# Optimization experiments

Measured on AMD Instinct MI355X. Metric: run time of the kernel, lower is better.

Reference implementation:

```python
import jax, jax.numpy as jnp
import numpy as np

B, ENC_LEN, DEC_LEN = 4, 1024, 256
ENC_H, DEC_H, ATTN = 1024, 1024, 256


def setup_inputs() -> dict:
    key = jax.random.key(0)
    k1, k2, k3, k4, k5, k6 = jax.random.split(key, 6)
    scale = 0.02
    return {
        "encoded_seq": jax.random.normal(k1, (B, ENC_LEN, ENC_H), jnp.float32),
        "decoder_state": jax.random.normal(k2, (B, DEC_LEN, DEC_H), jnp.float32),
        "input_pad_mask": jnp.ones((B, ENC_LEN), jnp.float32),
        "Wh": jax.random.normal(k3, (ENC_H, ATTN), jnp.float32) * scale,
        "Ws": jax.random.normal(k4, (DEC_H, ATTN), jnp.float32) * scale,
        "bs": jax.random.normal(k5, (ATTN,), jnp.float32) * scale,
        "v": jax.random.normal(k6, (ATTN,), jnp.float32) * scale,
    }


def reference(encoded_seq, decoder_state, input_pad_mask, Wh, Ws, bs, v):
    # projections: [B, dec, A] and [B, enc, A]
    proj_dec = jnp.einsum('bdh,ha->bda', decoder_state, Ws) + bs
    proj_enc = jnp.einsum('beh,ha->bea', encoded_seq, Wh)
    # additive score: tanh(broadcast add) then dot with selector vector v
    added = jnp.tanh(proj_dec[:, :, None, :] + proj_enc[:, None, :, :])  # [B,dec,enc,A]
    attn_logits = jnp.einsum('bdea,a->bde', added, v)                    # [B,dec,enc]
    attn_weights = jax.nn.softmax(attn_logits, axis=-1)
    attn_weights2 = attn_weights * input_pad_mask[:, None, :]
    attn_renorm = attn_weights2 / jnp.sum(attn_weights2, axis=-1, keepdims=True)
    context = jnp.einsum('bde,beh->bdh', attn_renorm, encoded_seq)       # [B,dec,enc_h]
    return context, attn_renorm
```

## Files before the change

### kernel.cpp

```cpp
#include <hip/hip_runtime.h>
#include <hip/hip_bf16.h>

#define BB 4
#define ENC_LEN 1024
#define DEC_LEN 256
#define ENC_H 1024
#define ATTN_A 256

#define C2F 2.8853900817779268f

typedef short bf16x8 __attribute__((ext_vector_type(8)));
typedef float f32x4 __attribute__((ext_vector_type(4)));
typedef unsigned int u32x2 __attribute__((ext_vector_type(2)));

union Q2D {
  uint4 q;
  u32x2 d[2];
};
union BF8 {
  u32x2 d[2];
  bf16x8 v;
};

static __device__ __forceinline__ unsigned short f2bf(float x) {
  union {
    float f;
    unsigned int u;
  } c;
  c.f = x;
  unsigned int r = c.u + 0x7FFFu + ((c.u >> 16) & 1u);
  return (unsigned short)(r >> 16);
}

__global__ __launch_bounds__(256) void prep_k(
    const float* __restrict__ Wh, const float* __restrict__ Ws,
    const float* __restrict__ enc, const float* __restrict__ dec,
    unsigned short* __restrict__ WhT, unsigned short* __restrict__ WsT,
    unsigned short* __restrict__ encT, unsigned short* __restrict__ encB,
    unsigned short* __restrict__ decB) {
  __shared__ unsigned short T[64][68];
  const int wb = blockIdx.x;
  const int t = threadIdx.x;
  const int lr = t >> 4;
  const int lc4 = (t & 15) * 4;

  if (wb >= 1152) {
    const int q = wb - 1152;
    const int r0 = (q >> 4) * 64;
    const int c0 = (q & 15) * 64;
#pragma unroll
    for (int p = 0; p < 4; ++p) {
      const int r = lr + p * 16;
      const float4 v = *(const float4*)&dec[(long)(r0 + r) * ENC_H + c0 + lc4];
      ushort4 o;
      o.x = f2bf(v.x);
      o.y = f2bf(v.y);
      o.z = f2bf(v.z);
      o.w = f2bf(v.w);
      *(ushort4*)&decB[(long)(r0 + r) * ENC_H + c0 + lc4] = o;
    }
    return;
  }

  const float* in;
  unsigned short* out;
  unsigned short* out2 = nullptr;
  int R, C, bx, by;
  if (wb < 128) {
    in = (wb < 64) ? Wh : Ws;
    out = (wb < 64) ? WhT : WsT;
    const int tt = wb & 63;
    R = ENC_H;
    C = ATTN_A;
    bx = tt & 3;
    by = tt >> 2;
  } else {
    const int tt0 = wb - 128;
    const int b = tt0 >> 8;
    const int tt = tt0 & 255;
    in = enc + (long)b * ENC_LEN * ENC_H;
    out = encT + (long)b * ENC_H * ENC_LEN;
    out2 = encB + (long)b * ENC_LEN * ENC_H;
    R = ENC_LEN;
    C = ENC_H;
    bx = tt & 15;
    by = tt >> 4;
  }
  const int r0 = by * 64;
  const int c0 = bx * 64;

#pragma unroll
  for (int p = 0; p < 4; ++p) {
    const int r = lr + p * 16;
    const float4 v = *(const float4*)&in[(long)(r0 + r) * C + c0 + lc4];
    ushort4 o;
    o.x = f2bf(v.x);
    o.y = f2bf(v.y);
    o.z = f2bf(v.z);
    o.w = f2bf(v.w);
    *(ushort4*)&T[r][lc4] = o;
    if (out2) *(ushort4*)&out2[(long)(r0 + r) * C + c0 + lc4] = o;
  }
  __syncthreads();
#pragma unroll
  for (int p = 0; p < 4; ++p) {
    const int c = lr + p * 16;
    ushort4 o;
    o.x = T[lc4 + 0][c];
    o.y = T[lc4 + 1][c];
    o.z = T[lc4 + 2][c];
    o.w = T[lc4 + 3][c];
    *(ushort4*)&out[(long)(c0 + c) * R + r0 + lc4] = o;
  }
}

__global__ __launch_bounds__(256) void pgemm(const unsigned short* __restrict__ decB,
                                             const unsigned short* __restrict__ encB,
                                             const unsigned short* __restrict__ WsT,
                                             const unsigned short* __restrict__ WhT,
                                             float* __restrict__ pdP,
                                             float* __restrict__ peP) {
  __shared__ unsigned short As[64][36];
  __shared__ unsigned short Bs[64][36];
  __shared__ float Cs[64][68];

  const int s = blockIdx.z;
  const bool isPD = blockIdx.y < 16;
  const unsigned short* A = isPD ? decB : encB;
  const unsigned short* BT = isPD ? WsT : WhT;
  const int m0 = (isPD ? blockIdx.y : (blockIdx.y - 16)) * 64;
  const int n0 = blockIdx.x * 64;
  const int kb = s * 512;

  const int tid = threadIdx.x;
  const int lane = tid & 63;
  const int wave = tid >> 6;
  const int quad = lane >> 4;
  const int l16 = lane & 15;
  const int wm = (wave >> 1) * 32;
  const int wn = (wave & 1) * 32;
  const int sr = tid >> 2;
  const int sk = (tid & 3) * 8;

  f32x4 acc[2][2] = {{{0.f, 0.f, 0.f, 0.f}, {0.f, 0.f, 0.f, 0.f}},
                     {{0.f, 0.f, 0.f, 0.f}, {0.f, 0.f, 0.f, 0.f}}};

  const unsigned short* Ap = A + (long)(m0 + sr) * ENC_H + kb + sk;
  const unsigned short* Bp = BT + (long)(n0 + sr) * ENC_H + kb + sk;

  Q2D av, bv;
  av.q = *(const uint4*)(Ap);
  bv.q = *(const uint4*)(Bp);

  for (int k0 = 0; k0 < 512; k0 += 32) {
    __syncthreads();
    *(u32x2*)&As[sr][sk] = av.d[0];
    *(u32x2*)&As[sr][sk + 4] = av.d[1];
    *(u32x2*)&Bs[sr][sk] = bv.d[0];
    *(u32x2*)&Bs[sr][sk + 4] = bv.d[1];
    const int kn = (k0 + 32 < 512) ? (k0 + 32) : 0;
    av.q = *(const uint4*)(Ap + kn);
    bv.q = *(const uint4*)(Bp + kn);
    __syncthreads();

    bf16x8 af[2], bfr[2];
#pragma unroll
    for (int i = 0; i < 2; ++i) {
      BF8 t;
      t.d[0] = *(const u32x2*)&As[wm + i * 16 + l16][quad * 8];
      t.d[1] = *(const u32x2*)&As[wm + i * 16 + l16][quad * 8 + 4];
      af[i] = t.v;
    }
#pragma unroll
    for (int j = 0; j < 2; ++j) {
      BF8 t;
      t.d[0] = *(const u32x2*)&Bs[wn + j * 16 + l16][quad * 8];
      t.d[1] = *(const u32x2*)&Bs[wn + j * 16 + l16][quad * 8 + 4];
      bfr[j] = t.v;
    }
#pragma unroll
    for (int i = 0; i < 2; ++i)
#pragma unroll
      for (int j = 0; j < 2; ++j)
        acc[i][j] = __builtin_amdgcn_mfma_f32_16x16x32_bf16(af[i], bfr[j], acc[i][j],
                                                            0, 0, 0);
  }

  if (isPD) {
    float* out = pdP + (long)s * (1024 * ATTN_A);
#pragma unroll
    for (int j = 0; j < 2; ++j) {
      const int col = n0 + wn + j * 16 + l16;
#pragma unroll
      for (int i = 0; i < 2; ++i) {
        const int row = m0 + wm + i * 16 + quad * 4;
#pragma unroll
        for (int r = 0; r < 4; ++r)
          out[(long)(row + r) * ATTN_A + col] = C2F * acc[i][j][r];
      }
    }
  } else {
    __syncthreads();
#pragma unroll
    for (int i = 0; i < 2; ++i)
#pragma unroll
      for (int j = 0; j < 2; ++j)
#pragma unroll
        for (int r = 0; r < 4; ++r)
          Cs[wn + j * 16 + l16][wm + i * 16 + quad * 4 + r] = C2F * acc[i][j][r];
    __syncthreads();
    const int gb = m0 >> 10;
    const int e0 = m0 & 1023;
    float* out = peP + (long)s * (BB * ATTN_A * ENC_LEN);
#pragma unroll
    for (int p = 0; p < 4; ++p) {
      const int arow = (tid >> 4) + p * 16;
      const int e4 = (tid & 15) * 4;
      const float4 o = *(const float4*)&Cs[arow][e4];
      *(float4*)&out[(long)gb * (ATTN_A * ENC_LEN) + (long)(n0 + arow) * ENC_LEN +
                     e0 + e4] = o;
    }
  }
}

__global__ __launch_bounds__(256) void logits_k(const float* __restrict__ peP,
                                                const float* __restrict__ pdP,
                                                const float* __restrict__ v,
                                                const float* __restrict__ bs,
                                                float* __restrict__ p0,
                                                float* __restrict__ p1) {
  const int tid = threadIdx.x;
  const int e = blockIdx.x * 256 + tid;
  const int d0 = blockIdx.y * 16;
  const int b = blockIdx.z >> 1;
  const int a0 = (blockIdx.z & 1) * 128;

  __shared__ float EdT[16][128];
  __shared__ float vv[128];

  {
    const int a = tid & 127;
    const int dh = tid >> 7;
    const float cb = C2F * bs[a0 + a];
#pragma unroll
    for (int j = 0; j < 8; ++j) {
      const int dd = dh * 8 + j;
      const long idx = (long)(b * DEC_LEN + d0 + dd) * ATTN_A + a0 + a;
      EdT[dd][a] =
          __builtin_amdgcn_exp2f(pdP[idx] + pdP[idx + 1024 * ATTN_A] + cb);
    }
    if (dh == 0) vv[a] = -2.0f * v[a0 + a];
  }
  __syncthreads();

  float acc[16];
#pragma unroll
  for (int i = 0; i < 16; ++i) acc[i] = 0.f;

  const float* pe0 = peP + (long)b * (ATTN_A * ENC_LEN) + (long)a0 * ENC_LEN + e;
  const float* pe1 = pe0 + (long)BB * ATTN_A * ENC_LEN;

  float pn0[4], pn1[4];
#pragma unroll
  for (int u = 0; u < 4; ++u) {
    pn0[u] = pe0[(long)u * ENC_LEN];
    pn1[u] = pe1[(long)u * ENC_LEN];
  }

  for (int a4 = 0; a4 < 128; a4 += 4) {
    float Ee[4];
#pragma unroll
    for (int u = 0; u < 4; ++u) Ee[u] = __builtin_amdgcn_exp2f(pn0[u] + pn1[u]);
    const int an = (a4 + 4 < 128) ? (a4 + 4) : 0;
#pragma unroll
    for (int u = 0; u < 4; ++u) {
      pn0[u] = pe0[(long)(an + u) * ENC_LEN];
      pn1[u] = pe1[(long)(an + u) * ENC_LEN];
    }
    const float4 v4 = *(const float4*)&vv[a4];

#pragma unroll
    for (int dd = 0; dd < 16; ++dd) {
      const float4 ed = *(const float4*)&EdT[dd][a4];
      const float dn0 = fmaf(ed.x, Ee[0], 1.0f);
      const float dn1 = fmaf(ed.y, Ee[1], 1.0f);
      const float dn2 = fmaf(ed.z, Ee[2], 1.0f);
      const float dn3 = fmaf(ed.w, Ee[3], 1.0f);
      const float x12 = dn0 * dn1;
      const float x34 = dn2 * dn3;
      float t1 = v4.x * dn1;
      t1 = fmaf(v4.y, dn0, t1);
      float t2 = v4.z * dn3;
      t2 = fmaf(v4.w, dn2, t2);
      float num = t1 * x34;
      num = fmaf(t2, x12, num);
      const float D = x12 * x34;
      const float r = __builtin_amdgcn_rcpf(D);
      acc[dd] = fmaf(num, r, acc[dd]);
    }
  }

  float* po = (blockIdx.z & 1) ? p1 : p0;
  const long base = ((long)(b * DEC_LEN + d0) * ENC_LEN) + e;
#pragma unroll
  for (int dd = 0; dd < 16; ++dd) po[base + (long)dd * ENC_LEN] = acc[dd];
}

__global__ __launch_bounds__(256) void softmax2_k(float* __restrict__ p0,
                                                  const float* __restrict__ p1,
                                                  const float* __restrict__ mask,
                                                  unsigned short* __restrict__ attnB) {
  const int row = blockIdx.x;
  const int b = row >> 8;
  const int tid = threadIdx.x;
  float* rp = p0 + (long)row * ENC_LEN;
  const float* rq = p1 + (long)row * ENC_LEN;
  const float* mp = mask + b * ENC_LEN;
  unsigned short* rb = attnB + (long)row * ENC_LEN;

  float l[4], m[4];
#pragma unroll
  for (int j = 0; j < 4; ++j) {
    l[j] = rp[tid + 256 * j] + rq[tid + 256 * j];
    m[j] = mp[tid + 256 * j];
  }

  __shared__ float redmax[4];
  __shared__ float redsum[4];
  const int lane = tid & 63;
  const int wid = tid >> 6;

  float tm = fmaxf(fmaxf(l[0], l[1]), fmaxf(l[2], l[3]));
#pragma unroll
  for (int off = 1; off < 64; off <<= 1) tm = fmaxf(tm, __shfl_xor(tm, off, 64));
  if (lane == 0) redmax[wid] = tm;
  __syncthreads();
  const float rmax = fmaxf(fmaxf(redmax[0], redmax[1]), fmaxf(redmax[2], redmax[3]));

  const float LOG2E = 1.4426950408889634f;
  float p[4];
  float ts = 0.f;
#pragma unroll
  for (int j = 0; j < 4; ++j) {
    p[j] = __builtin_amdgcn_exp2f((l[j] - rmax) * LOG2E) * m[j];
    ts += p[j];
  }
#pragma unroll
  for (int off = 1; off < 64; off <<= 1) ts += __shfl_xor(ts, off, 64);
  if (lane == 0) redsum[wid] = ts;
  __syncthreads();
  const float rsum = redsum[0] + redsum[1] + redsum[2] + redsum[3];

  const float inv = 1.0f / rsum;
#pragma unroll
  for (int j = 0; j < 4; ++j) {
    const float w = p[j] * inv;
    rp[tid + 256 * j] = w;
    rb[tid + 256 * j] = f2bf(w);
  }
}

__global__ __launch_bounds__(256) void cgemm(const unsigned short* __restrict__ attnB,
                                             const unsigned short* __restrict__ encT,
                                             float* __restrict__ cP) {
  __shared__ unsigned short As[64][36];
  __shared__ unsigned short Bs[64][36];

  const int b = blockIdx.z >> 1;
  const int s = blockIdx.z & 1;
  const int kb = s * 512;
  const unsigned short* A = attnB + (long)b * DEC_LEN * ENC_LEN;
  const unsigned short* BT = encT + (long)b * ENC_H * ENC_LEN;
  float* C = cP + (long)s * (BB * DEC_LEN * ENC_H) + (long)b * DEC_LEN * ENC_H;

  const int tid = threadIdx.x;
  const int lane = tid & 63;
  const int wave = tid >> 6;
  const int quad = lane >> 4;
  const int l16 = lane & 15;
  const int wm = (wave >> 1) * 32;
  const int wn = (wave & 1) * 32;
  const int m0 = blockIdx.y * 64;
  const int n0 = blockIdx.x * 64;
  const int sr = tid >> 2;
  const int sk = (tid & 3) * 8;

  f32x4 acc[2][2] = {{{0.f, 0.f, 0.f, 0.f}, {0.f, 0.f, 0.f, 0.f}},
                     {{0.f, 0.f, 0.f, 0.f}, {0.f, 0.f, 0.f, 0.f}}};

  const unsigned short* Ap = A + (long)(m0 + sr) * ENC_LEN + kb + sk;
  const unsigned short* Bp = BT + (long)(n0 + sr) * ENC_LEN + kb + sk;

  Q2D av, bv;
  av.q = *(const uint4*)(Ap);
  bv.q = *(const uint4*)(Bp);

  for (int k0 = 0; k0 < 512; k0 += 32) {
    __syncthreads();
    *(u32x2*)&As[sr][sk] = av.d[0];
    *(u32x2*)&As[sr][sk + 4] = av.d[1];
    *(u32x2*)&Bs[sr][sk] = bv.d[0];
    *(u32x2*)&Bs[sr][sk + 4] = bv.d[1];
    const int kn = (k0 + 32 < 512) ? (k0 + 32) : 0;
    av.q = *(const uint4*)(Ap + kn);
    bv.q = *(const uint4*)(Bp + kn);
    __syncthreads();

    bf16x8 af[2], bfr[2];
#pragma unroll
    for (int i = 0; i < 2; ++i) {
      BF8 t;
      t.d[0] = *(const u32x2*)&As[wm + i * 16 + l16][quad * 8];
      t.d[1] = *(const u32x2*)&As[wm + i * 16 + l16][quad * 8 + 4];
      af[i] = t.v;
    }
#pragma unroll
    for (int j = 0; j < 2; ++j) {
      BF8 t;
      t.d[0] = *(const u32x2*)&Bs[wn + j * 16 + l16][quad * 8];
      t.d[1] = *(const u32x2*)&Bs[wn + j * 16 + l16][quad * 8 + 4];
      bfr[j] = t.v;
    }
#pragma unroll
    for (int i = 0; i < 2; ++i)
#pragma unroll
      for (int j = 0; j < 2; ++j)
        acc[i][j] = __builtin_amdgcn_mfma_f32_16x16x32_bf16(af[i], bfr[j], acc[i][j],
                                                            0, 0, 0);
  }

#pragma unroll
  for (int j = 0; j < 2; ++j) {
    const int col = n0 + wn + j * 16 + l16;
#pragma unroll
    for (int i = 0; i < 2; ++i) {
      const int row = m0 + wm + i * 16 + quad * 4;
#pragma unroll
      for (int r = 0; r < 4; ++r) C[(long)(row + r) * ENC_H + col] = acc[i][j][r];
    }
  }
}

__global__ __launch_bounds__(256) void creduce(const float* __restrict__ cP,
                                               float* __restrict__ ctx) {
  const long i = ((long)blockIdx.x * 256 + threadIdx.x) * 4;
  const float4 x = *(const float4*)&cP[i];
  const float4 y = *(const float4*)&cP[i + (long)BB * DEC_LEN * ENC_H];
  float4 o;
  o.x = x.x + y.x;
  o.y = x.y + y.y;
  o.z = x.z + y.z;
  o.w = x.w + y.w;
  *(float4*)&ctx[i] = o;
}

template <int OMODE, bool BIAS>
__global__ __launch_bounds__(256) void gemm64(const float* __restrict__ A,
                                              const float* __restrict__ B,
                                              const float* __restrict__ bias,
                                              float* __restrict__ C,
                                              int K, int lda, int ldb, int ldc,
                                              long sA, long sB, long sC) {
  const int bz = blockIdx.z;
  A += (long)bz * sA;
  B += (long)bz * sB;
  C += (long)bz * sC;

  const int tid = threadIdx.x;
  const int tx = tid & 15;
  const int ty = tid >> 4;

  __shared__ float As2[16][64];
  __shared__ float Bs2[16][64];

  float acc[4][4];
#pragma unroll
  for (int i = 0; i < 4; ++i)
#pragma unroll
    for (int j = 0; j < 4; ++j) acc[i][j] = 0.f;

  const int ar = tid >> 2;
  const int ak4 = (tid & 3) << 2;
  const int br = tid >> 4;
  const int bn4 = (tid & 15) << 2;

  const float* Aload = A + (long)(blockIdx.y * 64 + ar) * lda + ak4;
  const float* Bload = B + (long)br * ldb + blockIdx.x * 64 + bn4;

  for (int k0 = 0; k0 < K; k0 += 16) {
    const float4 av = *(const float4*)(Aload + k0);
    const float4 bv = *(const float4*)(Bload + (long)k0 * ldb);
    __syncthreads();
    As2[ak4 + 0][ar] = av.x;
    As2[ak4 + 1][ar] = av.y;
    As2[ak4 + 2][ar] = av.z;
    As2[ak4 + 3][ar] = av.w;
    *(float4*)&Bs2[br][bn4] = bv;
    __syncthreads();
#pragma unroll
    for (int kk = 0; kk < 16; ++kk) {
      const float4 a4 = *(const float4*)&As2[kk][ty << 2];
      const float4 b4 = *(const float4*)&Bs2[kk][tx << 2];
      const float am[4] = {a4.x, a4.y, a4.z, a4.w};
      const float bn[4] = {b4.x, b4.y, b4.z, b4.w};
#pragma unroll
      for (int i = 0; i < 4; ++i)
#pragma unroll
        for (int j = 0; j < 4; ++j) acc[i][j] = fmaf(am[i], bn[j], acc[i][j]);
    }
  }

  if (OMODE == 0) {
    const int row0 = blockIdx.y * 64 + (ty << 2);
    const int col0 = blockIdx.x * 64 + (tx << 2);
    float4 bb4 = make_float4(0.f, 0.f, 0.f, 0.f);
    if (BIAS) bb4 = *(const float4*)&bias[col0];
#pragma unroll
    for (int i = 0; i < 4; ++i) {
      float4 o;
      o.x = acc[i][0] + bb4.x;
      o.y = acc[i][1] + bb4.y;
      o.z = acc[i][2] + bb4.z;
      o.w = acc[i][3] + bb4.w;
      *(float4*)&C[(long)(row0 + i) * ldc + col0] = o;
    }
  } else {
#pragma unroll
    for (int i = 0; i < 4; ++i) {
      const int gr = blockIdx.y * 64 + (ty << 2) + i;
      const int b = gr >> 10;
      const int e = gr & 1023;
#pragma unroll
      for (int j = 0; j < 4; ++j) {
        const int col = blockIdx.x * 64 + (tx << 2) + j;
        C[(long)b * (ATTN_A * ENC_LEN) + (long)col * ENC_LEN + e] = acc[i][j];
      }
    }
  }
}

__global__ __launch_bounds__(256) void logits_fb(const float* __restrict__ peT,
                                                 const float* __restrict__ pd,
                                                 const float* __restrict__ v,
                                                 float* __restrict__ out) {
  const int tid = threadIdx.x;
  const int e = blockIdx.x * 256 + tid;
  const int d0 = blockIdx.y * 8;
  const int b = blockIdx.z;

  __shared__ float cpd[ATTN_A][8];
  __shared__ float vv[ATTN_A];

  {
    const int a = tid;
#pragma unroll
    for (int dd = 0; dd < 8; ++dd)
      cpd[a][dd] = C2F * pd[((b * DEC_LEN + d0 + dd) * ATTN_A) + a];
    vv[a] = -2.0f * v[a];
  }
  __syncthreads();

  float acc[8] = {0.f, 0.f, 0.f, 0.f, 0.f, 0.f, 0.f, 0.f};
  const float* pe = peT + (long)b * (ATTN_A * ENC_LEN) + e;

  for (int a = 0; a < ATTN_A; a += 4) {
    float pes[4];
#pragma unroll
    for (int u = 0; u < 4; ++u) pes[u] = pe[(long)(a + u) * ENC_LEN];
#pragma unroll
    for (int u = 0; u < 4; ++u) {
      const float cpe = C2F * pes[u];
      const float vu = vv[a + u];
      const float4 c0 = *(const float4*)&cpd[a + u][0];
      const float4 c1 = *(const float4*)&cpd[a + u][4];
      const float cd[8] = {c0.x, c0.y, c0.z, c0.w, c1.x, c1.y, c1.z, c1.w};
#pragma unroll
      for (int dd = 0; dd < 8; ++dd) {
        const float x = cd[dd] + cpe;
        const float ex = __builtin_amdgcn_exp2f(x);
        const float r = __builtin_amdgcn_rcpf(ex + 1.0f);
        acc[dd] = fmaf(vu, r, acc[dd]);
      }
    }
  }

  const long base = ((long)(b * DEC_LEN + d0) * ENC_LEN) + e;
#pragma unroll
  for (int dd = 0; dd < 8; ++dd) out[base + (long)dd * ENC_LEN] = acc[dd];
}

__global__ __launch_bounds__(256) void softmax_fb(float* __restrict__ attn,
                                                  const float* __restrict__ mask) {
  const int row = blockIdx.x;
  const int b = row >> 8;
  const int tid = threadIdx.x;
  float* rp = attn + (long)row * ENC_LEN;
  const float* mp = mask + b * ENC_LEN;

  float l[4], m[4];
#pragma unroll
  for (int j = 0; j < 4; ++j) {
    l[j] = rp[tid + 256 * j];
    m[j] = mp[tid + 256 * j];
  }

  __shared__ float redmax[4];
  __shared__ float redsum[4];
  const int lane = tid & 63;
  const int wid = tid >> 6;

  float tm = fmaxf(fmaxf(l[0], l[1]), fmaxf(l[2], l[3]));
#pragma unroll
  for (int off = 1; off < 64; off <<= 1) tm = fmaxf(tm, __shfl_xor(tm, off, 64));
  if (lane == 0) redmax[wid] = tm;
  __syncthreads();
  const float rmax = fmaxf(fmaxf(redmax[0], redmax[1]), fmaxf(redmax[2], redmax[3]));

  const float LOG2E = 1.4426950408889634f;
  float p[4];
  float ts = 0.f;
#pragma unroll
  for (int j = 0; j < 4; ++j) {
    p[j] = __builtin_amdgcn_exp2f((l[j] - rmax) * LOG2E) * m[j];
    ts += p[j];
  }
#pragma unroll
  for (int off = 1; off < 64; off <<= 1) ts += __shfl_xor(ts, off, 64);
  if (lane == 0) redsum[wid] = ts;
  __syncthreads();
  const float rsum = redsum[0] + redsum[1] + redsum[2] + redsum[3];

  const float inv = 1.0f / rsum;
#pragma unroll
  for (int j = 0; j < 4; ++j) rp[tid + 256 * j] = p[j] * inv;
}

extern "C" void kernel_launch(void* const* d_in, const int* in_sizes, int n_in,
                              void* d_out, int out_size, void* d_ws, size_t ws_size,
                              hipStream_t stream) {
  const float* enc = (const float*)d_in[0];
  const float* dec = (const float*)d_in[1];
  const float* mask = (const float*)d_in[2];
  const float* Wh = (const float*)d_in[3];
  const float* Ws = (const float*)d_in[4];
  const float* bs = (const float*)d_in[5];
  const float* v = (const float*)d_in[6];

  float* ctx = (float*)d_out;
  float* attn = ctx + (long)BB * DEC_LEN * ENC_H;

  const long N_PD = 2L * 1024 * ATTN_A;
  const long N_PE = 2L * BB * ATTN_A * ENC_LEN;
  const long N_P1 = (long)BB * DEC_LEN * ENC_LEN;
  const long N_CP = 2L * BB * DEC_LEN * ENC_H;
  const long N_ENC = (long)BB * ENC_H * ENC_LEN;
  const long N_W = (long)ATTN_A * ENC_H;
  const long N_DEC = 1024L * ENC_H;
  const long N_ATT = (long)BB * DEC_LEN * ENC_LEN;
  const size_t FAST_WS = (N_PD + N_PE + N_P1 + N_CP) * 4 +
                         (N_ENC + 2 * N_W + N_ENC + N_DEC + N_ATT) * 2;

  if (ws_size >= FAST_WS) {
    float* pdP = (float*)d_ws;
    float* peP = pdP + N_PD;
    float* p1 = peP + N_PE;
    float* cP = p1 + N_P1;
    unsigned short* encT = (unsigned short*)(cP + N_CP);
    unsigned short* WhT = encT + N_ENC;
    unsigned short* WsT = WhT + N_W;
    unsigned short* encB = WsT + N_W;
    unsigned short* decB = encB + N_ENC;
    unsigned short* attnB = decB + N_DEC;

    prep_k<<<dim3(1408, 1, 1), 256, 0, stream>>>(Wh, Ws, enc, dec, WhT, WsT, encT,
                                                 encB, decB);
    pgemm<<<dim3(4, 80, 2), 256, 0, stream>>>(decB, encB, WsT, WhT, pdP, peP);
    logits_k<<<dim3(4, 16, BB * 2), 256, 0, stream>>>(peP, pdP, v, bs, attn, p1);
    softmax2_k<<<dim3(BB * DEC_LEN, 1, 1), 256, 0, stream>>>(attn, p1, mask, attnB);
    cgemm<<<dim3(16, 4, BB * 2), 256, 0, stream>>>(attnB, encT, cP);
    creduce<<<dim3(1024, 1, 1), 256, 0, stream>>>(cP, ctx);
  } else {
    float* pd = (float*)d_ws;
    float* peT = pd + (long)BB * DEC_LEN * ATTN_A;

    gemm64<0, true><<<dim3(ATTN_A / 64, (BB * DEC_LEN) / 64, 1), 256, 0, stream>>>(
        dec, Ws, bs, pd, ENC_H, ENC_H, ATTN_A, ATTN_A, 0, 0, 0);
    gemm64<1, false><<<dim3(ATTN_A / 64, (BB * ENC_LEN) / 64, 1), 256, 0, stream>>>(
        enc, Wh, nullptr, peT, ENC_H, ENC_H, ATTN_A, 0, 0, 0, 0);
    logits_fb<<<dim3(ENC_LEN / 256, DEC_LEN / 8, BB), 256, 0, stream>>>(peT, pd, v,
                                                                        attn);
    softmax_fb<<<dim3(BB * DEC_LEN, 1, 1), 256, 0, stream>>>(attn, mask);
    gemm64<0, false><<<dim3(ENC_H / 64, DEC_LEN / 64, BB), 256, 0, stream>>>(
        attn, enc, nullptr, ctx, ENC_LEN, ENC_LEN, ENC_H, ENC_H,
        (long)DEC_LEN * ENC_LEN, (long)ENC_LEN * ENC_H, (long)DEC_LEN * ENC_H);
  }
}
```

Baseline: 146.4 us.

## Split logits kernel over four attention-dim quarters with 8 decoder rows per block

The logits kernel now splits the attention dimension into four 64-wide slices instead of two 128-wide slices, and each block covers 8 decoder rows instead of 16. This quadruples the grid size to raise occupancy and latency hiding. The encoder-side prefetch is deepened to two stages. In exchange, there are four partial-logit buffers that the softmax kernel must read and sum, which adds workspace and memory traffic, and each block reuses its per-column exp values over fewer decoder rows.

```diff
diff --git a/kernel.cpp b/kernel.cpp
--- a/kernel.cpp
+++ b/kernel.cpp
@@ -228,23 +228,26 @@
                                                 const float* __restrict__ v,
                                                 const float* __restrict__ bs,
                                                 float* __restrict__ p0,
-                                                float* __restrict__ p1) {
+                                                float* __restrict__ p1,
+                                                float* __restrict__ p2,
+                                                float* __restrict__ p3) {
   const int tid = threadIdx.x;
   const int e = blockIdx.x * 256 + tid;
-  const int d0 = blockIdx.y * 16;
-  const int b = blockIdx.z >> 1;
-  const int a0 = (blockIdx.z & 1) * 128;
-
-  __shared__ float EdT[16][128];
-  __shared__ float vv[128];
+  const int d0 = blockIdx.y * 8;
+  const int b = blockIdx.z >> 2;
+  const int aq = blockIdx.z & 3;
+  const int a0 = aq * 64;
+
+  __shared__ float EdT[8][64];
+  __shared__ float vv[64];
 
   {
-    const int a = tid & 127;
-    const int dh = tid >> 7;
+    const int a = tid & 63;
+    const int dh = tid >> 6;
     const float cb = C2F * bs[a0 + a];
 #pragma unroll
-    for (int j = 0; j < 8; ++j) {
-      const int dd = dh * 8 + j;
+    for (int j = 0; j < 2; ++j) {
+      const int dd = dh * 2 + j;
       const long idx = (long)(b * DEC_LEN + d0 + dd) * ATTN_A + a0 + a;
       EdT[dd][a] =
           __builtin_amdgcn_exp2f(pdP[idx] + pdP[idx + 1024 * ATTN_A] + cb);
@@ -253,34 +256,35 @@
   }
   __syncthreads();
 
-  float acc[16];
-#pragma unroll
-  for (int i = 0; i < 16; ++i) acc[i] = 0.f;
-
+  float acc[8] = {0.f, 0.f, 0.f, 0.f, 0.f, 0.f, 0.f, 0.f};
   const float* pe0 = peP + (long)b * (ATTN_A * ENC_LEN) + (long)a0 * ENC_LEN + e;
   const float* pe1 = pe0 + (long)BB * ATTN_A * ENC_LEN;
 
-  float pn0[4], pn1[4];
+  float pA0[4], pA1[4], pB0[4], pB1[4];
 #pragma unroll
   for (int u = 0; u < 4; ++u) {
-    pn0[u] = pe0[(long)u * ENC_LEN];
-    pn1[u] = pe1[(long)u * ENC_LEN];
-  }
-
-  for (int a4 = 0; a4 < 128; a4 += 4) {
+    pA0[u] = pe0[(long)u * ENC_LEN];
+    pA1[u] = pe1[(long)u * ENC_LEN];
+    pB0[u] = pe0[(long)(4 + u) * ENC_LEN];
+    pB1[u] = pe1[(long)(4 + u) * ENC_LEN];
+  }
+
+  for (int a4 = 0; a4 < 64; a4 += 4) {
     float Ee[4];
 #pragma unroll
-    for (int u = 0; u < 4; ++u) Ee[u] = __builtin_amdgcn_exp2f(pn0[u] + pn1[u]);
-    const int an = (a4 + 4 < 128) ? (a4 + 4) : 0;
+    for (int u = 0; u < 4; ++u) Ee[u] = __builtin_amdgcn_exp2f(pA0[u] + pA1[u]);
+    const int an = (a4 + 8 < 64) ? (a4 + 8) : 0;
 #pragma unroll
     for (int u = 0; u < 4; ++u) {
-      pn0[u] = pe0[(long)(an + u) * ENC_LEN];
-      pn1[u] = pe1[(long)(an + u) * ENC_LEN];
+      pA0[u] = pB0[u];
+      pA1[u] = pB1[u];
+      pB0[u] = pe0[(long)(an + u) * ENC_LEN];
+      pB1[u] = pe1[(long)(an + u) * ENC_LEN];
     }
     const float4 v4 = *(const float4*)&vv[a4];
 
 #pragma unroll
-    for (int dd = 0; dd < 16; ++dd) {
+    for (int dd = 0; dd < 8; ++dd) {
       const float4 ed = *(const float4*)&EdT[dd][a4];
       const float dn0 = fmaf(ed.x, Ee[0], 1.0f);
       const float dn1 = fmaf(ed.y, Ee[1], 1.0f);
@@ -300,29 +304,34 @@
     }
   }
 
-  float* po = (blockIdx.z & 1) ? p1 : p0;
+  float* po = (aq == 0) ? p0 : (aq == 1) ? p1 : (aq == 2) ? p2 : p3;
   const long base = ((long)(b * DEC_LEN + d0) * ENC_LEN) + e;
 #pragma unroll
-  for (int dd = 0; dd < 16; ++dd) po[base + (long)dd * ENC_LEN] = acc[dd];
-}
-
-__global__ __launch_bounds__(256) void softmax2_k(float* __restrict__ p0,
+  for (int dd = 0; dd < 8; ++dd) po[base + (long)dd * ENC_LEN] = acc[dd];
+}
+
+__global__ __launch_bounds__(256) void softmax4_k(float* __restrict__ p0,
                                                   const float* __restrict__ p1,
+                                                  const float* __restrict__ p2,
+                                                  const float* __restrict__ p3,
                                                   const float* __restrict__ mask,
                                                   unsigned short* __restrict__ attnB) {
   const int row = blockIdx.x;
   const int b = row >> 8;
   const int tid = threadIdx.x;
   float* rp = p0 + (long)row * ENC_LEN;
-  const float* rq = p1 + (long)row * ENC_LEN;
+  const float* rq1 = p1 + (long)row * ENC_LEN;
+  const float* rq2 = p2 + (long)row * ENC_LEN;
+  const float* rq3 = p3 + (long)row * ENC_LEN;
   const float* mp = mask + b * ENC_LEN;
   unsigned short* rb = attnB + (long)row * ENC_LEN;
 
   float l[4], m[4];
 #pragma unroll
   for (int j = 0; j < 4; ++j) {
-    l[j] = rp[tid + 256 * j] + rq[tid + 256 * j];
-    m[j] = mp[tid + 256 * j];
+    const int i = tid + 256 * j;
+    l[j] = (rp[i] + rq1[i]) + (rq2[i] + rq3[i]);
+    m[j] = mp[i];
   }
 
   __shared__ float redmax[4];
@@ -657,14 +666,16 @@
   const long N_W = (long)ATTN_A * ENC_H;
   const long N_DEC = 1024L * ENC_H;
   const long N_ATT = (long)BB * DEC_LEN * ENC_LEN;
-  const size_t FAST_WS = (N_PD + N_PE + N_P1 + N_CP) * 4 +
+  const size_t FAST_WS = (N_PD + N_PE + 3 * N_P1 + N_CP) * 4 +
                          (N_ENC + 2 * N_W + N_ENC + N_DEC + N_ATT) * 2;
 
   if (ws_size >= FAST_WS) {
     float* pdP = (float*)d_ws;
     float* peP = pdP + N_PD;
     float* p1 = peP + N_PE;
-    float* cP = p1 + N_P1;
+    float* p2 = p1 + N_P1;
+    float* p3 = p2 + N_P1;
+    float* cP = p3 + N_P1;
     unsigned short* encT = (unsigned short*)(cP + N_CP);
     unsigned short* WhT = encT + N_ENC;
     unsigned short* WsT = WhT + N_W;
@@ -675,8 +686,10 @@
     prep_k<<<dim3(1408, 1, 1), 256, 0, stream>>>(Wh, Ws, enc, dec, WhT, WsT, encT,
                                                  encB, decB);
     pgemm<<<dim3(4, 80, 2), 256, 0, stream>>>(decB, encB, WsT, WhT, pdP, peP);
-    logits_k<<<dim3(4, 16, BB * 2), 256, 0, stream>>>(peP, pdP, v, bs, attn, p1);
-    softmax2_k<<<dim3(BB * DEC_LEN, 1, 1), 256, 0, stream>>>(attn, p1, mask, attnB);
+    logits_k<<<dim3(4, 32, BB * 4), 256, 0, stream>>>(peP, pdP, v, bs, attn, p1, p2,
+                                                      p3);
+    softmax4_k<<<dim3(BB * DEC_LEN, 1, 1), 256, 0, stream>>>(attn, p1, p2, p3, mask,
+                                                             attnB);
     cgemm<<<dim3(16, 4, BB * 2), 256, 0, stream>>>(attnB, encT, cP);
     creduce<<<dim3(1024, 1, 1), 256, 0, stream>>>(cP, ctx);
   } else {
```

After: 146.6 us. About the same (+0.1%).
